# Kernel tuning notes

Measured on AMD Instinct MI355X. Metric: run time of the kernel, lower is better.

The kernel has to match this reference:

```python
import jax, jax.numpy as jnp
import numpy as np

B, T, DIN, H = 8, 512, 256, 512
D = 2 * H            # d_model = 1024
HEADS, DH, DEPTH, M = 8, 128, 2, 256  # M = nb_features
FF = 4 * D
KEPS = 1e-4          # performer kernel epsilon


def setup_inputs() -> dict:
    key = jax.random.key(0)
    ks = iter(jax.random.split(key, 64))
    def nrm(shape, s=1.0):
        return jax.random.normal(next(ks), shape, jnp.float32) * s
    inp = {"x": nrm((B, T, DIN))}
    # BiLSTM params, stacked over direction [2, ...]; torch gate order i,f,g,o
    for l, din in ((0, DIN), (1, D)):
        s = 1.0 / np.sqrt(H)
        inp[f"l{l}_Wih"] = nrm((2, 4 * H, din), s)
        inp[f"l{l}_Whh"] = nrm((2, 4 * H, H), s)
        inp[f"l{l}_bih"] = nrm((2, 4 * H), s)
        inp[f"l{l}_bhh"] = nrm((2, 4 * H), s)
    # FAVOR+ random projection (buffer), [nb_features, dim_head]
    inp["proj"] = nrm((M, DH))
    sd = 1.0 / np.sqrt(D)
    inp["ln1_g"] = jnp.ones((DEPTH, D)); inp["ln1_b"] = jnp.zeros((DEPTH, D))
    for n in ("Wq", "Wk", "Wv", "Wo"):
        inp[n] = nrm((DEPTH, D, D), sd)
    for n in ("bq", "bk", "bv", "bo"):
        inp[n] = jnp.zeros((DEPTH, D))
    inp["ln2_g"] = jnp.ones((DEPTH, D)); inp["ln2_b"] = jnp.zeros((DEPTH, D))
    inp["Wf1"] = nrm((DEPTH, D, FF), sd); inp["bf1"] = jnp.zeros((DEPTH, FF))
    inp["Wf2"] = nrm((DEPTH, FF, D), 1.0 / np.sqrt(FF)); inp["bf2"] = jnp.zeros((DEPTH, D))
    inp["cW1"] = nrm((D, H), sd); inp["cb1"] = jnp.zeros((H,))
    inp["cW2"] = nrm((H, 2), 1.0 / np.sqrt(H)); inp["cb2"] = jnp.zeros((2,))
    return inp


def _lstm_dir(x, Wih, Whh, bih, bhh, reverse):
    xs = jnp.swapaxes(x, 0, 1)                      # [T,B,Din]
    h0 = jnp.zeros((x.shape[0], H), x.dtype)
    def step(carry, xt):
        h, c = carry
        z = xt @ Wih.T + h @ Whh.T + bih + bhh      # [B,4H]
        i, f, g, o = jnp.split(z, 4, axis=-1)
        c = jax.nn.sigmoid(f) * c + jax.nn.sigmoid(i) * jnp.tanh(g)
        h = jax.nn.sigmoid(o) * jnp.tanh(c)
        return (h, c), h
    _, hs = jax.lax.scan(step, (h0, h0), xs, reverse=reverse)
    return jnp.swapaxes(hs, 0, 1)                   # [B,T,H], time-aligned


def _bilstm(x, Wih, Whh, bih, bhh):
    fwd = _lstm_dir(x, Wih[0], Whh[0], bih[0], bhh[0], False)
    bwd = _lstm_dir(x, Wih[1], Whh[1], bih[1], bhh[1], True)
    return jnp.concatenate([fwd, bwd], axis=-1)     # [B,T,2H]


def _ln(x, g, b):
    mu = jnp.mean(x, -1, keepdims=True)
    v = jnp.mean((x - mu) ** 2, -1, keepdims=True)
    return (x - mu) * jax.lax.rsqrt(v + 1e-5) * g + b


def _favor(data, proj, is_query):
    # softmax_kernel of performer-pytorch (eval mode, fixed projection)
    dn = DH ** -0.25
    dd = jnp.einsum('bhnd,md->bhnm', data * dn, proj)
    diag = jnp.sum(data * data, -1) * (dn * dn * 0.5)      # [b,h,n]
    if is_query:
        mx = jnp.max(dd, axis=-1, keepdims=True)
    else:
        mx = jnp.max(dd, axis=(-1, -2), keepdims=True)
    return (jnp.exp(dd - diag[..., None] - mx) + KEPS) * (M ** -0.5)


def _heads(x, W, b):
    return (x @ W + b).reshape(B, T, HEADS, DH).transpose(0, 2, 1, 3)


def reference(x, l0_Wih, l0_Whh, l0_bih, l0_bhh, l1_Wih, l1_Whh, l1_bih, l1_bhh,
              proj, ln1_g, ln1_b, Wq, bq, Wk, bk, Wv, bv, Wo, bo,
              ln2_g, ln2_b, Wf1, bf1, Wf2, bf2, cW1, cb1, cW2, cb2):
    h = _bilstm(x, l0_Wih, l0_Whh, l0_bih, l0_bhh)
    h = _bilstm(h, l1_Wih, l1_Whh, l1_bih, l1_bhh)          # [B,T,D]
    for i in range(DEPTH):
        # pre-norm FAVOR+ self-attention, non-causal linear attention
        y = _ln(h, ln1_g[i], ln1_b[i])
        q = _favor(_heads(y, Wq[i], bq[i]), proj, True)     # [b,h,n,m]
        k = _favor(_heads(y, Wk[i], bk[i]), proj, False)
        v = _heads(y, Wv[i], bv[i])                         # [b,h,n,d]
        dinv = 1.0 / jnp.einsum('bhnm,bhm->bhn', q, k.sum(axis=2))
        ctx = jnp.einsum('bhnm,bhnd->bhmd', k, v)
        o = jnp.einsum('bhnm,bhmd->bhnd', q, ctx) * dinv[..., None]
        o = o.transpose(0, 2, 1, 3).reshape(B, T, D)
        h = h + (o @ Wo[i] + bo[i])
        # pre-norm feedforward (GELU, mult 4)
        y = _ln(h, ln2_g[i], ln2_b[i])
        h = h + (jax.nn.gelu(y @ Wf1[i] + bf1[i], approximate=False) @ Wf2[i] + bf2[i])
    pooled = h.mean(axis=1)                                 # [B,D]
    logits = jax.nn.relu(pooled @ cW1 + cb1) @ cW2 + cb2    # [B,2]
    return logits
```

## Files before the change

### kernel.cpp

```cpp
#include <hip/hip_runtime.h>

#define KEPS 1e-4f

typedef __attribute__((ext_vector_type(8))) short bf16x8;
typedef __attribute__((ext_vector_type(4))) float f32x4;
typedef __attribute__((ext_vector_type(4))) unsigned u32x4;
typedef unsigned short u16;

__device__ float g_z0[2u*512*2048*8];
__device__ float g_z1[2u*512*2048*8];
__device__ float g_hres[8u*512*1024];
__device__ float g_qlin[8u*8*512*128];
__device__ float g_klin[8u*8*512*128];
__device__ float g_vlin[8u*8*512*128];
__device__ float g_qp[8u*8*512*256];
__device__ float g_ddb[8u*8*512*256];
__device__ float g_kT[8u*8*256*512];
__device__ float g_ctx[64u*256*128];
__device__ float g_bs0[2*2048];
__device__ float g_bs1[2*2048];
__device__ float g_diagq[32768];
__device__ float g_diagk[32768];
__device__ float g_kmx[64];
__device__ float g_ksum[64*256];
__device__ float g_dinv[32768];
__device__ __align__(16) unsigned g_hbuf[2*2*8*256];
__device__ float g_pooled[8*1024];

__device__ u16 g_xbf[8u*512*256];
__device__ u16 g_x1bf[8u*512*1024];
__device__ u16 g_ybf[8u*512*1024];
__device__ u16 g_ylo[8u*512*1024];
__device__ u16 g_obufbf[8u*512*1024];
__device__ u16 g_ffbbf[8u*512*4096];
__device__ u16 g_qhi[8u*8*512*128];
__device__ u16 g_qlo2[8u*8*512*128];
__device__ u16 g_khi[8u*8*512*128];
__device__ u16 g_klo2[8u*8*512*128];
__device__ u16 g_wih0b[2u*2048*256];
__device__ u16 g_wih1b[2u*2048*1024];
__device__ u16 g_wvt[2u*1024*1024];
__device__ u16 g_wot[2u*1024*1024];
__device__ u16 g_wf1t[2u*4096*1024];
__device__ u16 g_wf2t[2u*1024*4096];
__device__ u16 g_wqth[2u*1024*1024];
__device__ u16 g_wqtl[2u*1024*1024];
__device__ u16 g_wkth[2u*1024*1024];
__device__ u16 g_wktl[2u*1024*1024];
__device__ u16 g_projh[256*128];
__device__ u16 g_projl[256*128];

__device__ __forceinline__ float gelu_f(float x) {
  return 0.5f * x * (1.f + erff(x * 0.70710678118654752f));
}
__device__ __forceinline__ unsigned f2bf(float f) {
  unsigned x = __float_as_uint(f);
  return (x + 0x7FFFu + ((x >> 16) & 1u)) >> 16;
}
__device__ __forceinline__ float bf2f(unsigned h) {
  return __uint_as_float(h << 16);
}
__device__ __forceinline__ u32x4 ld16_sc1(const unsigned* p) {
  u32x4 v;
  asm volatile("global_load_dwordx4 %0, %1, off sc1\n\ts_waitcnt vmcnt(0)"
               : "=v"(v) : "v"(p) : "memory");
  return v;
}
__device__ __forceinline__ void st16_sc1(unsigned* p, u32x4 v) {
  asm volatile("global_store_dwordx4 %0, %1, off sc1" :: "v"(p), "v"(v) : "memory");
}

__global__ void k_add2(float* __restrict__ dst, const float* __restrict__ a,
                       const float* __restrict__ b, int n) {
  int i = blockIdx.x * 256 + threadIdx.x;
  if (i < n) dst[i] = a[i] + b[i];
}
__global__ void k_cvt(const float* __restrict__ src, u16* __restrict__ dst, int n4) {
  int i = blockIdx.x * 256 + threadIdx.x;
  if (i < n4) {
    float4 v = ((const float4*)src)[i];
    ushort4 o; o.x=(u16)f2bf(v.x); o.y=(u16)f2bf(v.y); o.z=(u16)f2bf(v.z); o.w=(u16)f2bf(v.w);
    ((ushort4*)dst)[i] = o;
  }
}
__global__ void k_scale_split(const float* __restrict__ a, u16* __restrict__ dh,
                              u16* __restrict__ dl, float s, int n) {
  int i = blockIdx.x*256 + threadIdx.x;
  if (i < n) {
    float v = a[i]*s;
    unsigned h = f2bf(v);
    dh[i] = (u16)h; dl[i] = (u16)f2bf(v - bf2f(h));
  }
}
__global__ void k_w2bfT(const float* __restrict__ src, u16* __restrict__ dst,
                        int K, int N, long long sBS, long long dBS)
{
  __shared__ float tile[32][33];
  const int z = blockIdx.z;
  const int n0 = blockIdx.x*32, k0 = blockIdx.y*32;
  const int tx = threadIdx.x, ty = threadIdx.y;
  const float* s = src + (long long)z*sBS;
  u16* d = dst + (long long)z*dBS;
  #pragma unroll
  for (int j = 0; j < 4; ++j)
    tile[ty + j*8][tx] = s[(long long)(k0 + ty + j*8)*N + n0 + tx];
  __syncthreads();
  #pragma unroll
  for (int j = 0; j < 4; ++j)
    d[(long long)(n0 + ty + j*8)*K + k0 + tx] = (u16)f2bf(tile[tx][ty + j*8]);
}
__global__ void k_w2bfT_split(const float* __restrict__ src, u16* __restrict__ dh,
                              u16* __restrict__ dl, int K, int N,
                              long long sBS, long long dBS)
{
  __shared__ float tile[32][33];
  const int z = blockIdx.z;
  const int n0 = blockIdx.x*32, k0 = blockIdx.y*32;
  const int tx = threadIdx.x, ty = threadIdx.y;
  const float* s = src + (long long)z*sBS;
  #pragma unroll
  for (int j = 0; j < 4; ++j)
    tile[ty + j*8][tx] = s[(long long)(k0 + ty + j*8)*N + n0 + tx];
  __syncthreads();
  #pragma unroll
  for (int j = 0; j < 4; ++j) {
    const float v = tile[tx][ty + j*8];
    const unsigned h = f2bf(v);
    const long long off = (long long)z*dBS + (long long)(n0 + ty + j*8)*K + k0 + tx;
    dh[off] = (u16)h; dl[off] = (u16)f2bf(v - bf2f(h));
  }
}

template<int MODE>
__global__ __launch_bounds__(256)
void k_bgemm(const u16* __restrict__ A, const u16* __restrict__ Bw,
             const float* __restrict__ bias, void* __restrict__ Cv,
             int Ndim, int Kdim,
             long long aBS, long long bBS, long long cBS, long long biasBS)
{
  __shared__ __align__(16) u16 As[128*40];
  __shared__ __align__(16) u16 Bs[128*40];
  const int tid = threadIdx.x;
  const int m0 = blockIdx.y * 128, n0 = blockIdx.x * 128, z = blockIdx.z;
  const u16* Ab = A + (long long)z*aBS;
  const u16* Bb = Bw + (long long)z*bBS;
  const int wv = tid >> 6, l = tid & 63;
  const int wm = wv >> 1, wn = wv & 1;
  const int lr = l & 15, lk = l >> 4;
  const int str = tid >> 2, stc = (tid & 3)*8;
  f32x4 acc[4][4];
  #pragma unroll
  for (int i=0;i<4;++i)
    #pragma unroll
    for (int j=0;j<4;++j) acc[i][j] = (f32x4){0.f,0.f,0.f,0.f};

  for (int k0 = 0; k0 < Kdim; k0 += 32) {
    #pragma unroll
    for (int q = 0; q < 2; ++q) {
      const int r = q*64 + str;
      *(uint4*)&As[r*40 + stc] = *(const uint4*)&Ab[(long long)(m0 + r)*Kdim + k0 + stc];
      *(uint4*)&Bs[r*40 + stc] = *(const uint4*)&Bb[(long long)(n0 + r)*Kdim + k0 + stc];
    }
    __syncthreads();
    bf16x8 af[4], bfr[4];
    #pragma unroll
    for (int i=0;i<4;++i) af[i]  = *(bf16x8*)&As[(wm*64 + i*16 + lr)*40 + lk*8];
    #pragma unroll
    for (int j=0;j<4;++j) bfr[j] = *(bf16x8*)&Bs[(wn*64 + j*16 + lr)*40 + lk*8];
    #pragma unroll
    for (int i=0;i<4;++i)
      #pragma unroll
      for (int j=0;j<4;++j)
        acc[i][j] = __builtin_amdgcn_mfma_f32_16x16x32_bf16(af[i], bfr[j], acc[i][j], 0, 0, 0);
    __syncthreads();
  }

  #pragma unroll
  for (int j=0;j<4;++j) {
    const int n = n0 + wn*64 + j*16 + lr;
    const float bvv = bias ? bias[(long long)z*biasBS + n] : 0.f;
    #pragma unroll
    for (int i=0;i<4;++i) {
      #pragma unroll
      for (int r=0;r<4;++r) {
        const int m = m0 + wm*64 + i*16 + lk*4 + r;
        float v = acc[i][j][r] + bvv;
        if (MODE == 0) {
          ((float*)Cv)[(long long)z*cBS + (long long)m*Ndim + n] = v;
        } else if (MODE == 1) {
          const int b_ = m >> 9, t_ = m & 511;
          ((float*)Cv)[(long long)z*cBS + ((long long)t_*2048 + n)*8 + b_] = v;
        } else if (MODE == 2) {
          const int b_ = m >> 9, t_ = m & 511;
          const int hd = n >> 7;
          ((float*)Cv)[(((long long)(b_*8 + hd))*512 + t_)*128 + (n & 127)] = v;
        } else if (MODE == 3) {
          float* cp = (float*)Cv + (long long)m*Ndim + n;
          *cp += v;
        } else if (MODE == 4) {
          ((u16*)Cv)[(long long)m*Ndim + n] = (u16)f2bf(gelu_f(v));
        }
      }
    }
  }
}

template<int MODE>
__global__ __launch_bounds__(256)
void k_b3gemm(const u16* __restrict__ Ah, const u16* __restrict__ Al,
              const u16* __restrict__ Bh, const u16* __restrict__ Bl,
              const float* __restrict__ bias, float* __restrict__ Cf,
              u16* __restrict__ Chi, u16* __restrict__ Clo,
              int Ndim, int Kdim)
{
  __shared__ __align__(16) u16 Ash[128*40];
  __shared__ __align__(16) u16 Asl[128*40];
  __shared__ __align__(16) u16 Bsh[128*40];
  __shared__ __align__(16) u16 Bsl[128*40];
  const int tid = threadIdx.x;
  const int m0 = blockIdx.y * 128, n0 = blockIdx.x * 128;
  const int wv = tid >> 6, l = tid & 63;
  const int wm = wv >> 1, wn = wv & 1;
  const int lr = l & 15, lk = l >> 4;
  const int str = tid >> 2, stc = (tid & 3)*8;
  f32x4 acc[4][4];
  #pragma unroll
  for (int i=0;i<4;++i)
    #pragma unroll
    for (int j=0;j<4;++j) acc[i][j] = (f32x4){0.f,0.f,0.f,0.f};

  for (int k0 = 0; k0 < Kdim; k0 += 32) {
    #pragma unroll
    for (int q = 0; q < 2; ++q) {
      const int r = q*64 + str;
      const long long ao = (long long)(m0 + r)*Kdim + k0 + stc;
      const long long bo = (long long)(n0 + r)*Kdim + k0 + stc;
      *(uint4*)&Ash[r*40 + stc] = *(const uint4*)&Ah[ao];
      *(uint4*)&Asl[r*40 + stc] = *(const uint4*)&Al[ao];
      *(uint4*)&Bsh[r*40 + stc] = *(const uint4*)&Bh[bo];
      *(uint4*)&Bsl[r*40 + stc] = *(const uint4*)&Bl[bo];
    }
    __syncthreads();
    bf16x8 ah[4], al_[4], bh[4], bl_[4];
    #pragma unroll
    for (int i=0;i<4;++i) {
      ah[i]  = *(bf16x8*)&Ash[(wm*64 + i*16 + lr)*40 + lk*8];
      al_[i] = *(bf16x8*)&Asl[(wm*64 + i*16 + lr)*40 + lk*8];
    }
    #pragma unroll
    for (int j=0;j<4;++j) {
      bh[j]  = *(bf16x8*)&Bsh[(wn*64 + j*16 + lr)*40 + lk*8];
      bl_[j] = *(bf16x8*)&Bsl[(wn*64 + j*16 + lr)*40 + lk*8];
    }
    #pragma unroll
    for (int i=0;i<4;++i)
      #pragma unroll
      for (int j=0;j<4;++j) {
        acc[i][j] = __builtin_amdgcn_mfma_f32_16x16x32_bf16(ah[i],  bh[j],  acc[i][j], 0, 0, 0);
        acc[i][j] = __builtin_amdgcn_mfma_f32_16x16x32_bf16(ah[i],  bl_[j], acc[i][j], 0, 0, 0);
        acc[i][j] = __builtin_amdgcn_mfma_f32_16x16x32_bf16(al_[i], bh[j],  acc[i][j], 0, 0, 0);
      }
    __syncthreads();
  }

  #pragma unroll
  for (int j=0;j<4;++j) {
    const int n = n0 + wn*64 + j*16 + lr;
    const float bvv = bias ? bias[n] : 0.f;
    #pragma unroll
    for (int i=0;i<4;++i) {
      #pragma unroll
      for (int r=0;r<4;++r) {
        const int m = m0 + wm*64 + i*16 + lk*4 + r;
        float v = acc[i][j][r] + bvv;
        if (MODE == 0) {
          Cf[(long long)m*Ndim + n] = v;
        } else if (MODE == 2) {
          const int b_ = m >> 9, t_ = m & 511;
          const int hd = n >> 7;
          const long long off = (((long long)(b_*8 + hd))*512 + t_)*128 + (n & 127);
          Cf[off] = v;
          const unsigned h = f2bf(v);
          Chi[off] = (u16)h;
          Clo[off] = (u16)f2bf(v - bf2f(h));
        }
      }
    }
  }
}

template<int BT, int MODE>
__global__ __launch_bounds__(256)
void k_gemm(const float* __restrict__ A, const float* __restrict__ Bw,
            const float* __restrict__ bias, float* __restrict__ C,
            int Mdim, int Ndim, int Kdim,
            long long aBS, long long bBS, long long cBS, long long biasBS,
            const float* __restrict__ aux)
{
  __shared__ float As[16][128];
  __shared__ float Bs[16][128];
  const int tid = threadIdx.x;
  const int tx = tid & 15, ty = tid >> 4;
  const int m0 = blockIdx.y * 128, n0 = blockIdx.x * 128;
  const int z = blockIdx.z;
  const float* Ab = A + (long long)z * aBS;
// ... 20 lines not shown
      #pragma unroll
      for (int l0 = 0; l0 < 512; l0 += 256) {
        const int ll = l0 + tid;
        const int kr = ll >> 5, n4 = (ll & 31) * 4;
        *(float4*)&Bs[kr][n4] = *(const float4*)&Bb[(long long)(k0 + kr) * Ndim + n0 + n4];
      }
    }
    __syncthreads();
    #pragma unroll
    for (int kk = 0; kk < 16; ++kk) {
      float4 af0 = *(const float4*)&As[kk][ty*4];
      float4 af1 = *(const float4*)&As[kk][64 + ty*4];
      float4 bf0 = *(const float4*)&Bs[kk][tx*4];
      float4 bf1 = *(const float4*)&Bs[kk][64 + tx*4];
      float av[8] = {af0.x,af0.y,af0.z,af0.w,af1.x,af1.y,af1.z,af1.w};
      float bv[8] = {bf0.x,bf0.y,bf0.z,bf0.w,bf1.x,bf1.y,bf1.z,bf1.w};
      #pragma unroll
      for (int i = 0; i < 8; ++i)
        #pragma unroll
        for (int j = 0; j < 8; ++j)
          acc[i][j] = fmaf(av[i], bv[j], acc[i][j]);
    }
    __syncthreads();
  }

  float* Cz = C + (long long)z * cBS;
  #pragma unroll
  for (int i = 0; i < 8; ++i) {
    const int m = m0 + ((i < 4) ? (ty*4 + i) : (64 + ty*4 + (i - 4)));
    #pragma unroll
    for (int jb = 0; jb < 2; ++jb) {
      const int ci = n0 + (jb ? 64 : 0) + tx*4;
      float4 v;
      v.x = acc[i][jb*4+0]; v.y = acc[i][jb*4+1];
      v.z = acc[i][jb*4+2]; v.w = acc[i][jb*4+3];
      if (MODE == 0) {
        *(float4*)&Cz[(long long)m * Ndim + ci] = v;
      } else if (MODE == 5) {
        const int b_ = z >> 3, hd = z & 7;
        const float sc = aux[(long long)z*512 + m];
        u16* Cb = (u16*)C;
        const long long off = ((long long)(b_*512 + m))*1024 + hd*128 + ci;
        Cb[off+0] = (u16)f2bf(v.x*sc);
        Cb[off+1] = (u16)f2bf(v.y*sc);
        Cb[off+2] = (u16)f2bf(v.z*sc);
        Cb[off+3] = (u16)f2bf(v.w*sc);
      }
    }
  }
}

template<int OBF>
__global__ __launch_bounds__(512)
void k_lstm5(const float* __restrict__ Z, const float* __restrict__ Whh,
             float* __restrict__ outf, u16* __restrict__ outb,
             unsigned* __restrict__ hbufU)
{
  extern __shared__ char smem[];
  short*          Wl    = (short*)smem;
  short*          hl    = (short*)(smem + 131072);
  float*          gates = (float*)(smem + 139264);
  unsigned short* houts = (unsigned short*)(smem + 143360);

  const int slice = blockIdx.x & 15, dir = blockIdx.x >> 4;
  const int tid = threadIdx.x;
  const int u0 = slice * 32;

  for (int blk = tid; blk < 8192; blk += 512) {
    const int lr2 = blk >> 6, bi = blk & 63;
    const long long src = ((long long)dir*2048 + (lr2>>5)*512 + u0 + (lr2&31))*512 + bi*8;
    float4 w0 = *(const float4*)&Whh[src];
    float4 w1 = *(const float4*)&Whh[src + 4];
    unsigned* dst = (unsigned*)&Wl[lr2*512 + (((bi + lr2) & 63) << 3)];
    dst[0] = f2bf(w0.x) | (f2bf(w0.y) << 16);
    dst[1] = f2bf(w0.z) | (f2bf(w0.w) << 16);
    dst[2] = f2bf(w1.x) | (f2bf(w1.y) << 16);
    dst[3] = f2bf(w1.z) | (f2bf(w1.w) << 16);
  }
  for (int i = tid; i < 2048; i += 512) ((unsigned*)hl)[i] = 0u;

  const int wv = tid >> 6, l = tid & 63;
  const int arow = wv*16 + (l & 15);
  const int bb   = l & 7;
  const int qoff = l >> 4;
  const int jj = tid >> 3, bcomb = tid & 7;
  float cst = 0.f;
  int gt = 1;
  int pt = 2;

  for (int s = 0; s < 512; ++s) {
    const int t = dir ? (511 - s) : s;
    float z0v = 0.f, z1v = 0.f, z2v = 0.f, z3v = 0.f;
    if (tid < 256) {
      const float* zp = Z + (((long long)dir*512 + t)*16384) + (u0 + jj)*8 + bcomb;
      z0v = zp[0]; z1v = zp[4096]; z2v = zp[8192]; z3v = zp[12288];
    }
    if (s > 0) {
      const unsigned base = ((unsigned)((s & 1)*2 + dir)) * 2048;
      const unsigned* src = &hbufU[base + tid*4];
      u32x4 v;
      for (;;) {
        v = ld16_sc1(src);
        const int tag = (int)((v.x & 1u) | (((v.x >> 16) & 1u) << 1) | ((v.y & 1u) << 2));
        if (tag == gt) break;
      }
      const int b = tid >> 6, q = tid & 63;
      *(u32x4*)((char*)hl + b*1024 + (((q + b) & 63) << 4)) = v;
    }
    __syncthreads();
    f32x4 acc0 = {0.f,0.f,0.f,0.f}, acc1 = {0.f,0.f,0.f,0.f};
    #pragma unroll
    for (int ks = 0; ks < 8; ++ks) {
      const int qa = (2*ks)*4 + qoff, qb = (2*ks + 1)*4 + qoff;
      bf16x8 a0 = *(bf16x8*)&Wl[arow*512 + (((qa + arow) & 63) << 3)];
      bf16x8 b0 = *(bf16x8*)&hl[bb*512   + (((qa + bb)   & 63) << 3)];
      acc0 = __builtin_amdgcn_mfma_f32_16x16x32_bf16(a0, b0, acc0, 0, 0, 0);
      bf16x8 a1 = *(bf16x8*)&Wl[arow*512 + (((qb + arow) & 63) << 3)];
      bf16x8 b1 = *(bf16x8*)&hl[bb*512   + (((qb + bb)   & 63) << 3)];
      acc1 = __builtin_amdgcn_mfma_f32_16x16x32_bf16(a1, b1, acc1, 0, 0, 0);
    }
    const int bcol = l & 15;
    if (bcol < 8) {
      #pragma unroll
      for (int r = 0; r < 4; ++r)
        gates[(wv*16 + qoff*4 + r)*8 + bcol] = acc0[r] + acc1[r];
    }
    __syncthreads();
    if (tid < 256) {
      const float gi = gates[jj*8        + bcomb] + z0v;
      const float gf = gates[(32+jj)*8   + bcomb] + z1v;
      const float gg = gates[(64+jj)*8   + bcomb] + z2v;
      const float go = gates[(96+jj)*8   + bcomb] + z3v;
      const float ig = 1.f/(1.f + expf(-gi));
      const float fg = 1.f/(1.f + expf(-gf));
      const float og = 1.f/(1.f + expf(-go));
      cst = fg*cst + ig*tanhf(gg);
      const float hv = og*tanhf(cst);
      const unsigned hb = f2bf(hv);
      if (OBF) outb[((long long)(bcomb*512 + t))*1024 + (dir<<9) + u0 + jj] = (u16)hb;
      else     outf[((long long)(bcomb*512 + t))*1024 + (dir<<9) + u0 + jj] = hv;
      houts[bcomb*32 + jj] = (unsigned short)hb;
    }
    __syncthreads();
    if (s != 511 && tid < 32) {
      const int b = tid >> 2, q4 = tid & 3;
      u32x4 w = *(const u32x4*)&houts[b*32 + q4*8];
      w.x = (w.x & ~0x00010001u) | (unsigned)(pt & 1) | (((unsigned)(pt >> 1) & 1u) << 16);
      w.y = (w.y & ~1u) | ((unsigned)(pt >> 2) & 1u);
      const unsigned base2 = ((unsigned)(((s+1) & 1)*2 + dir)) * 2048;
      st16_sc1(&hbufU[base2 + b*256 + (u0 >> 1) + q4*4], w);
    }
    gt = (gt == 7) ? 1 : gt + 1;
    pt = (pt == 7) ? 1 : pt + 1;
  }
}

__global__ __launch_bounds__(256)
void k_ln(const float* __restrict__ X, const float* __restrict__ gw,
          const float* __restrict__ bw, u16* __restrict__ Yh, u16* __restrict__ Yl)
{
  const int row = blockIdx.x, tid = threadIdx.x;
  const float* xr = X + (long long)row * 1024;
  float4 v = *(const float4*)&xr[tid*4];
  float s  = v.x + v.y + v.z + v.w;
  float ss = v.x*v.x + v.y*v.y + v.z*v.z + v.w*v.w;
  #pragma unroll
  for (int off = 1; off < 64; off <<= 1) {
    s  += __shfl_xor(s, off, 64);
    ss += __shfl_xor(ss, off, 64);
  }
  __shared__ float rs[4], rss[4];
  const int w = tid >> 6;
  if ((tid & 63) == 0) { rs[w] = s; rss[w] = ss; }
  __syncthreads();
  s  = rs[0] + rs[1] + rs[2] + rs[3];
  ss = rss[0] + rss[1] + rss[2] + rss[3];
  const float mu = s * (1.f/1024.f);
  const float var = ss * (1.f/1024.f) - mu*mu;
  const float rstd = rsqrtf(var + 1e-5f);
  float4 g4 = *(const float4*)&gw[tid*4];
  float4 b4 = *(const float4*)&bw[tid*4];
  float4 o;
  o.x = (v.x - mu)*rstd*g4.x + b4.x;
  o.y = (v.y - mu)*rstd*g4.y + b4.y;
  o.z = (v.z - mu)*rstd*g4.z + b4.z;
  o.w = (v.w - mu)*rstd*g4.w + b4.w;
  ushort4 hh, ll;
  hh.x=(u16)f2bf(o.x); ll.x=(u16)f2bf(o.x - bf2f(f2bf(o.x)));
  hh.y=(u16)f2bf(o.y); ll.y=(u16)f2bf(o.y - bf2f(f2bf(o.y)));
  hh.z=(u16)f2bf(o.z); ll.z=(u16)f2bf(o.z - bf2f(f2bf(o.z)));
  hh.w=(u16)f2bf(o.w); ll.w=(u16)f2bf(o.w - bf2f(f2bf(o.w)));
  *(ushort4*)&Yh[(long long)row*1024 + tid*4] = hh;
  *(ushort4*)&Yl[(long long)row*1024 + tid*4] = ll;
}

__global__ void k_diag(const float* __restrict__ X, float* __restrict__ dout)
{
  const int tid = threadIdx.x;
  const int row = blockIdx.x*4 + (tid >> 6);
  const int lane = tid & 63;
  float2 v = *(const float2*)&X[(long long)row*128 + lane*2];
  float ss = v.x*v.x + v.y*v.y;
  #pragma unroll
  for (int off = 1; off < 64; off <<= 1) ss += __shfl_xor(ss, off, 64);
  if (lane == 0) dout[row] = ss * 0.044194173824159216f;
}

// ... 152 lines not shown
  const float* ln2b  = (const float*)d_in[21];
  const float* Wf1   = (const float*)d_in[22];
  const float* bf1   = (const float*)d_in[23];
  const float* Wf2   = (const float*)d_in[24];
  const float* bf2   = (const float*)d_in[25];
  const float* cW1   = (const float*)d_in[26];
  const float* cb1   = (const float*)d_in[27];
  const float* cW2   = (const float*)d_in[28];
  const float* cb2   = (const float*)d_in[29];

  float* z0    = (float*)symp(HIP_SYMBOL(g_z0));
  float* z1    = (float*)symp(HIP_SYMBOL(g_z1));
  float* hres  = (float*)symp(HIP_SYMBOL(g_hres));
  float* qlin  = (float*)symp(HIP_SYMBOL(g_qlin));
  float* klin  = (float*)symp(HIP_SYMBOL(g_klin));
  float* vlin  = (float*)symp(HIP_SYMBOL(g_vlin));
  float* qp    = (float*)symp(HIP_SYMBOL(g_qp));
  float* ddb   = (float*)symp(HIP_SYMBOL(g_ddb));
  float* kT    = (float*)symp(HIP_SYMBOL(g_kT));
  float* ctx   = (float*)symp(HIP_SYMBOL(g_ctx));
  float* bs0   = (float*)symp(HIP_SYMBOL(g_bs0));
  float* bs1   = (float*)symp(HIP_SYMBOL(g_bs1));
  float* diagq = (float*)symp(HIP_SYMBOL(g_diagq));
  float* diagk = (float*)symp(HIP_SYMBOL(g_diagk));
  float* kmx   = (float*)symp(HIP_SYMBOL(g_kmx));
  float* ksum  = (float*)symp(HIP_SYMBOL(g_ksum));
  float* dinv  = (float*)symp(HIP_SYMBOL(g_dinv));
  unsigned* hbuf = (unsigned*)symp(HIP_SYMBOL(g_hbuf));
  float* pooled= (float*)symp(HIP_SYMBOL(g_pooled));
  u16* xbf   = (u16*)symp(HIP_SYMBOL(g_xbf));
  u16* x1bf  = (u16*)symp(HIP_SYMBOL(g_x1bf));
  u16* ybf   = (u16*)symp(HIP_SYMBOL(g_ybf));
  u16* ylo   = (u16*)symp(HIP_SYMBOL(g_ylo));
  u16* obufbf= (u16*)symp(HIP_SYMBOL(g_obufbf));
  u16* ffbbf = (u16*)symp(HIP_SYMBOL(g_ffbbf));
  u16* qhi   = (u16*)symp(HIP_SYMBOL(g_qhi));
  u16* qlo2  = (u16*)symp(HIP_SYMBOL(g_qlo2));
  u16* khi   = (u16*)symp(HIP_SYMBOL(g_khi));
  u16* klo2  = (u16*)symp(HIP_SYMBOL(g_klo2));
  u16* wih0b = (u16*)symp(HIP_SYMBOL(g_wih0b));
  u16* wih1b = (u16*)symp(HIP_SYMBOL(g_wih1b));
  u16* wvt   = (u16*)symp(HIP_SYMBOL(g_wvt));
  u16* wot   = (u16*)symp(HIP_SYMBOL(g_wot));
  u16* wf1t  = (u16*)symp(HIP_SYMBOL(g_wf1t));
  u16* wf2t  = (u16*)symp(HIP_SYMBOL(g_wf2t));
  u16* wqth  = (u16*)symp(HIP_SYMBOL(g_wqth));
  u16* wqtl  = (u16*)symp(HIP_SYMBOL(g_wqtl));
  u16* wkth  = (u16*)symp(HIP_SYMBOL(g_wkth));
  u16* wktl  = (u16*)symp(HIP_SYMBOL(g_wktl));
  u16* projh = (u16*)symp(HIP_SYMBOL(g_projh));
  u16* projl = (u16*)symp(HIP_SYMBOL(g_projl));

  const float dn = 0.29730177875068026f;
  const int LSTM_LDS = 143872;
  (void)hipFuncSetAttribute((const void*)k_lstm5<1>,
                            hipFuncAttributeMaxDynamicSharedMemorySize, LSTM_LDS);
  (void)hipFuncSetAttribute((const void*)k_lstm5<0>,
                            hipFuncAttributeMaxDynamicSharedMemorySize, LSTM_LDS);

  k_add2<<<16, 256, 0, stream>>>(bs0, l0bih, l0bhh, 4096);
  k_add2<<<16, 256, 0, stream>>>(bs1, l1bih, l1bhh, 4096);
  k_scale_split<<<128, 256, 0, stream>>>(proj, projh, projl, dn, 32768);

  k_cvt<<<1024, 256, 0, stream>>>(x, xbf, 262144);
  k_cvt<<<1024, 256, 0, stream>>>(l0Wih, wih0b, 262144);
  k_cvt<<<4096, 256, 0, stream>>>(l1Wih, wih1b, 1048576);
  k_w2bfT<<<dim3(32,32,2),  dim3(32,8), 0, stream>>>(Wv,  wvt,  1024, 1024, 1048576LL, 1048576LL);
  k_w2bfT<<<dim3(32,32,2),  dim3(32,8), 0, stream>>>(Wo,  wot,  1024, 1024, 1048576LL, 1048576LL);
  k_w2bfT<<<dim3(128,32,2), dim3(32,8), 0, stream>>>(Wf1, wf1t, 1024, 4096, 4194304LL, 4194304LL);
  k_w2bfT<<<dim3(32,128,2), dim3(32,8), 0, stream>>>(Wf2, wf2t, 4096, 1024, 4194304LL, 4194304LL);
  k_w2bfT_split<<<dim3(32,32,2), dim3(32,8), 0, stream>>>(Wq, wqth, wqtl, 1024, 1024, 1048576LL, 1048576LL);
  k_w2bfT_split<<<dim3(32,32,2), dim3(32,8), 0, stream>>>(Wk, wkth, wktl, 1024, 1024, 1048576LL, 1048576LL);

  k_bgemm<1><<<dim3(16,32,2), 256, 0, stream>>>(xbf, wih0b, bs0, z0,
      2048, 256, 0LL, 524288LL, 8388608LL, 2048LL);
  k_lstm5<1><<<32, 512, LSTM_LDS, stream>>>(z0, l0Whh, nullptr, x1bf, hbuf);
  k_bgemm<1><<<dim3(16,32,2), 256, 0, stream>>>(x1bf, wih1b, bs1, z1,
      2048, 1024, 0LL, 2097152LL, 8388608LL, 2048LL);
  k_lstm5<0><<<32, 512, LSTM_LDS, stream>>>(z1, l1Whh, hres, nullptr, hbuf);

  for (int i = 0; i < 2; ++i) {
    const long long wOffU = (long long)i * 1048576;
    k_ln<<<4096, 256, 0, stream>>>(hres, ln1g + i*1024, ln1b + i*1024, ybf, ylo);
    k_b3gemm<2><<<dim3(8,32,1), 256, 0, stream>>>(ybf, ylo, wqth + wOffU, wqtl + wOffU,
        bq + i*1024, qlin, qhi, qlo2, 1024, 1024);
    k_b3gemm<2><<<dim3(8,32,1), 256, 0, stream>>>(ybf, ylo, wkth + wOffU, wktl + wOffU,
        bk + i*1024, klin, khi, klo2, 1024, 1024);
    k_bgemm<2><<<dim3(8,32,1), 256, 0, stream>>>(ybf, wvt + wOffU, bv + i*1024, vlin,
        1024, 1024, 0LL, 0LL, 0LL, 0LL);
    k_diag<<<8192, 256, 0, stream>>>(qlin, diagq);
    k_diag<<<8192, 256, 0, stream>>>(klin, diagk);
    k_b3gemm<0><<<dim3(2,256,1), 256, 0, stream>>>(qhi, qlo2, projh, projl,
        nullptr, qp, nullptr, nullptr, 256, 128);
    k_favq<<<8192, 256, 0, stream>>>(qp, diagq);
    k_b3gemm<0><<<dim3(2,256,1), 256, 0, stream>>>(khi, klo2, projh, projl,
        nullptr, ddb, nullptr, nullptr, 256, 128);
    k_kmax<<<64, 256, 0, stream>>>(ddb, kmx);
    k_fkT<<<dim3(16,8,64), dim3(32,8), 0, stream>>>(ddb, diagk, kmx, kT);
    k_ksum<<<4096, 256, 0, stream>>>(kT, ksum);
    k_gemm<0,0><<<dim3(1,2,64), 256, 0, stream>>>(kT, vlin, nullptr, ctx,
        256, 128, 512, 131072LL, 65536LL, 32768LL, 0LL, nullptr);
    k_dinv<<<8192, 256, 0, stream>>>(qp, ksum, dinv);
    k_gemm<0,5><<<dim3(1,4,64), 256, 0, stream>>>(qp, ctx, nullptr, (float*)obufbf,
        512, 128, 256, 131072LL, 32768LL, 0LL, 0LL, dinv);
    k_bgemm<3><<<dim3(8,32,1), 256, 0, stream>>>(obufbf, wot + wOffU, bo + i*1024, hres,
        1024, 1024, 0LL, 0LL, 0LL, 0LL);
    k_ln<<<4096, 256, 0, stream>>>(hres, ln2g + i*1024, ln2b + i*1024, ybf, ylo);
    k_bgemm<4><<<dim3(32,32,1), 256, 0, stream>>>(ybf, wf1t + (long long)i*4194304,
        bf1 + i*4096, ffbbf, 4096, 1024, 0LL, 0LL, 0LL, 0LL);
    k_bgemm<3><<<dim3(8,32,1), 256, 0, stream>>>(ffbbf, wf2t + (long long)i*4194304,
        bf2 + i*1024, hres, 1024, 4096, 0LL, 0LL, 0LL, 0LL);
  }

  k_pool<<<32, 256, 0, stream>>>(hres, pooled);
  k_cls<<<8, 256, 0, stream>>>(pooled, cW1, cb1, cW2, cb2, (float*)d_out);
}
```

Baseline: 4.362 ms.

## Split LSTM batch into two halves to overlap h exchange with MFMA

The recurrent LSTM kernel now splits the 8 batch columns into two groups of 4, each with its own LDS h buffer and its own global exchange slot. While one half's gate matmul and cell update run, the other half's hidden state load from peer blocks is already in flight. The z loads and h loads are issued early with raw asm and waited on with explicit vmcnt counts, and plain s_barrier replaces __syncthreads. This is meant to hide cross-block communication latency on the serial time chain, at the cost of doubling the MFMA passes, which now use half-empty operands, and of fragile hand-managed waitcnt ordering.

```diff
diff --git a/kernel.cpp b/kernel.cpp
--- a/kernel.cpp
+++ b/kernel.cpp
@@ -24,7 +24,7 @@
 __device__ float g_kmx[64];
 __device__ float g_ksum[64*256];
 __device__ float g_dinv[32768];
-__device__ __align__(16) unsigned g_hbuf[2*2*8*256];
+__device__ __align__(16) unsigned g_hbuf[2*2*2*1024];
 __device__ float g_pooled[8*1024];
 
 __device__ u16 g_xbf[8u*512*256];
@@ -66,8 +66,20 @@
                : "=v"(v) : "v"(p) : "memory");
   return v;
 }
+__device__ __forceinline__ void ld16_sc1_issue(u32x4& v, const unsigned* p) {
+  asm volatile("global_load_dwordx4 %0, %1, off sc1" : "=v"(v) : "v"(p));
+}
+__device__ __forceinline__ void ld4_issue(float& d, const float* p) {
+  asm volatile("global_load_dword %0, %1, off" : "=v"(d) : "v"(p));
+}
 __device__ __forceinline__ void st16_sc1(unsigned* p, u32x4 v) {
   asm volatile("global_store_dwordx4 %0, %1, off sc1" :: "v"(p), "v"(v) : "memory");
+}
+__device__ __forceinline__ void bar_raw() {
+  asm volatile("s_waitcnt lgkmcnt(0)" ::: "memory");
+  __builtin_amdgcn_sched_barrier(0);
+  __builtin_amdgcn_s_barrier();
+  __builtin_amdgcn_sched_barrier(0);
 }
 
 __global__ void k_add2(float* __restrict__ dst, const float* __restrict__ a,
@@ -377,15 +389,15 @@
 
 template<int OBF>
 __global__ __launch_bounds__(512)
-void k_lstm5(const float* __restrict__ Z, const float* __restrict__ Whh,
+void k_lstm6(const float* __restrict__ Z, const float* __restrict__ Whh,
              float* __restrict__ outf, u16* __restrict__ outb,
              unsigned* __restrict__ hbufU)
 {
   extern __shared__ char smem[];
-  short*          Wl    = (short*)smem;
-  short*          hl    = (short*)(smem + 131072);
-  float*          gates = (float*)(smem + 139264);
-  unsigned short* houts = (unsigned short*)(smem + 143360);
+  short* Wl    = (short*)smem;
+  char*  hlA   = smem + 131072;
+  char*  hlB   = smem + 135168;
+  float* gates = (float*)(smem + 139264);
 
   const int slice = blockIdx.x & 15, dir = blockIdx.x >> 4;
   const int tid = threadIdx.x;
@@ -402,82 +414,166 @@
     dst[2] = f2bf(w1.x) | (f2bf(w1.y) << 16);
     dst[3] = f2bf(w1.z) | (f2bf(w1.w) << 16);
   }
-  for (int i = tid; i < 2048; i += 512) ((unsigned*)hl)[i] = 0u;
+  for (int i = tid; i < 2048; i += 512) {
+    ((unsigned*)hlA)[i & 1023] = 0u;
+    ((unsigned*)hlB)[(i >> 1) & 1023] = 0u;
+  }
+  for (int i = tid; i < 1024; i += 512) { ((unsigned*)hlA)[i] = 0u; ((unsigned*)hlB)[i] = 0u; }
 
   const int wv = tid >> 6, l = tid & 63;
   const int arow = wv*16 + (l & 15);
-  const int bb   = l & 7;
+  const int bbop = l & 3;
   const int qoff = l >> 4;
-  const int jj = tid >> 3, bcomb = tid & 7;
+  const int cidx = tid & 127, jjc = cidx >> 2, bloc = cidx & 3;
+  const int isA = (tid < 128), isB = (tid >= 128 && tid < 256);
+  const int batch = isA ? bloc : 4 + bloc;
+  const int q4 = 2*((cidx >> 6) & 1) + ((l >> 5) & 1);
   float cst = 0.f;
   int gt = 1;
   int pt = 2;
+  u32x4 vA = {0,0,0,0}, vB = {0,0,0,0};
+
+  const int dirbase = dir * 2;
 
   for (int s = 0; s < 512; ++s) {
     const int t = dir ? (511 - s) : s;
-    float z0v = 0.f, z1v = 0.f, z2v = 0.f, z3v = 0.f;
+    float z0v=0.f, z1v=0.f, z2v=0.f, z3v=0.f;
+    const float* zp = Z + (((long long)dir*512 + t)*16384) + (u0 + jjc)*8 + batch;
     if (tid < 256) {
-      const float* zp = Z + (((long long)dir*512 + t)*16384) + (u0 + jj)*8 + bcomb;
-      z0v = zp[0]; z1v = zp[4096]; z2v = zp[8192]; z3v = zp[12288];
-    }
-    if (s > 0) {
-      const unsigned base = ((unsigned)((s & 1)*2 + dir)) * 2048;
-      const unsigned* src = &hbufU[base + tid*4];
-      u32x4 v;
-      for (;;) {
-        v = ld16_sc1(src);
-        const int tag = (int)((v.x & 1u) | (((v.x >> 16) & 1u) << 1) | ((v.y & 1u) << 2));
-        if (tag == gt) break;
+      ld4_issue(z0v, zp);
+      ld4_issue(z1v, zp + 4096);
+      ld4_issue(z2v, zp + 8192);
+      ld4_issue(z3v, zp + 12288);
+    }
+    const unsigned* adA = hbufU + (((s & 1)*2 + dir)*2 + 0)*1024 + tid*4;
+    if (s > 0 && tid < 256) {
+      asm volatile("s_waitcnt vmcnt(4)" : "+v"(vA));
+      int tag = (int)((vA.x & 1u) | (((vA.x >> 16) & 1u) << 1) | ((vA.y & 1u) << 2));
+      while (tag != gt) {
+        vA = ld16_sc1(adA);
+        tag = (int)((vA.x & 1u) | (((vA.x >> 16) & 1u) << 1) | ((vA.y & 1u) << 2));
       }
       const int b = tid >> 6, q = tid & 63;
-      *(u32x4*)((char*)hl + b*1024 + (((q + b) & 63) << 4)) = v;
-    }
-    __syncthreads();
-    f32x4 acc0 = {0.f,0.f,0.f,0.f}, acc1 = {0.f,0.f,0.f,0.f};
-    #pragma unroll
-    for (int ks = 0; ks < 8; ++ks) {
-      const int qa = (2*ks)*4 + qoff, qb = (2*ks + 1)*4 + qoff;
-      bf16x8 a0 = *(bf16x8*)&Wl[arow*512 + (((qa + arow) & 63) << 3)];
-      bf16x8 b0 = *(bf16x8*)&hl[bb*512   + (((qa + bb)   & 63) << 3)];
-      acc0 = __builtin_amdgcn_mfma_f32_16x16x32_bf16(a0, b0, acc0, 0, 0, 0);
-      bf16x8 a1 = *(bf16x8*)&Wl[arow*512 + (((qb + arow) & 63) << 3)];
-      bf16x8 b1 = *(bf16x8*)&hl[bb*512   + (((qb + bb)   & 63) << 3)];
-      acc1 = __builtin_amdgcn_mfma_f32_16x16x32_bf16(a1, b1, acc1, 0, 0, 0);
-    }
-    const int bcol = l & 15;
-    if (bcol < 8) {
+      *(u32x4*)(hlA + b*1024 + (((q + b) & 63) << 4)) = vA;
+    }
+    const unsigned* adB = hbufU + (((s & 1)*2 + dir)*2 + 1)*1024 + tid*4;
+    if (s > 0 && tid < 256) ld16_sc1_issue(vB, adB);
+    bar_raw();
+    {
+      f32x4 acc0 = {0.f,0.f,0.f,0.f}, acc1 = {0.f,0.f,0.f,0.f};
       #pragma unroll
-      for (int r = 0; r < 4; ++r)
-        gates[(wv*16 + qoff*4 + r)*8 + bcol] = acc0[r] + acc1[r];
-    }
-    __syncthreads();
-    if (tid < 256) {
-      const float gi = gates[jj*8        + bcomb] + z0v;
-      const float gf = gates[(32+jj)*8   + bcomb] + z1v;
-      const float gg = gates[(64+jj)*8   + bcomb] + z2v;
-      const float go = gates[(96+jj)*8   + bcomb] + z3v;
+      for (int ks = 0; ks < 8; ++ks) {
+        const int qa = (2*ks)*4 + qoff, qb = (2*ks + 1)*4 + qoff;
+        bf16x8 a0 = *(bf16x8*)&Wl[arow*512 + (((qa + arow) & 63) << 3)];
+        bf16x8 b0 = *(bf16x8*)(hlA + bbop*1024 + (((qa + bbop) & 63) << 4));
+        acc0 = __builtin_amdgcn_mfma_f32_16x16x32_bf16(a0, b0, acc0, 0, 0, 0);
+        bf16x8 a1 = *(bf16x8*)&Wl[arow*512 + (((qb + arow) & 63) << 3)];
+        bf16x8 b1 = *(bf16x8*)(hlA + bbop*1024 + (((qb + bbop) & 63) << 4));
+        acc1 = __builtin_amdgcn_mfma_f32_16x16x32_bf16(a1, b1, acc1, 0, 0, 0);
+      }
+      const int bcol = l & 15;
+      if (bcol < 4) {
+        #pragma unroll
+        for (int r = 0; r < 4; ++r)
+          gates[(wv*16 + qoff*4 + r)*4 + bcol] = acc0[r] + acc1[r];
+      }
+    }
+    bar_raw();
+    if (isA) {
+      if (s == 0) { asm volatile("s_waitcnt vmcnt(0)" : "+v"(z0v), "+v"(z1v), "+v"(z2v), "+v"(z3v)); }
+      else        { asm volatile("s_waitcnt vmcnt(1)" : "+v"(z0v), "+v"(z1v), "+v"(z2v), "+v"(z3v)); }
+      const float gi = gates[jjc*4 + bloc]        + z0v;
+      const float gf = gates[(32+jjc)*4 + bloc]   + z1v;
+      const float gg = gates[(64+jjc)*4 + bloc]   + z2v;
+      const float go = gates[(96+jjc)*4 + bloc]   + z3v;
       const float ig = 1.f/(1.f + expf(-gi));
       const float fg = 1.f/(1.f + expf(-gf));
       const float og = 1.f/(1.f + expf(-go));
       cst = fg*cst + ig*tanhf(gg);
       const float hv = og*tanhf(cst);
       const unsigned hb = f2bf(hv);
-      if (OBF) outb[((long long)(bcomb*512 + t))*1024 + (dir<<9) + u0 + jj] = (u16)hb;
-      else     outf[((long long)(bcomb*512 + t))*1024 + (dir<<9) + u0 + jj] = hv;
-      houts[bcomb*32 + jj] = (unsigned short)hb;
-    }
-    __syncthreads();
-    if (s != 511 && tid < 32) {
-      const int b = tid >> 2, q4 = tid & 3;
-      u32x4 w = *(const u32x4*)&houts[b*32 + q4*8];
-      w.x = (w.x & ~0x00010001u) | (unsigned)(pt & 1) | (((unsigned)(pt >> 1) & 1u) << 16);
-      w.y = (w.y & ~1u) | ((unsigned)(pt >> 2) & 1u);
-      const unsigned base2 = ((unsigned)(((s+1) & 1)*2 + dir)) * 2048;
-      st16_sc1(&hbufU[base2 + b*256 + (u0 >> 1) + q4*4], w);
+      if (OBF) outb[((long long)(batch*512 + t))*1024 + (dir<<9) + u0 + jjc] = (u16)hb;
+      else     outf[((long long)(batch*512 + t))*1024 + (dir<<9) + u0 + jjc] = hv;
+      unsigned p  = hb | (((unsigned)__shfl_down((int)hb, 4)) << 16);
+      unsigned q0 = p, q1 = (unsigned)__shfl_down((int)p, 8);
+      unsigned r2 = (unsigned)__shfl_down((int)q0, 16), r3 = (unsigned)__shfl_down((int)q1, 16);
+      if (s != 511 && (l & 28) == 0) {
+        u32x4 w;
+        w.x = (q0 & ~0x00010001u) | (unsigned)(pt & 1) | (((unsigned)(pt >> 1) & 1u) << 16);
+        w.y = (q1 & ~1u) | ((unsigned)(pt >> 2) & 1u);
+        w.z = r2; w.w = r3;
+        unsigned* pa = hbufU + ((((s+1) & 1)*2 + dir)*2 + 0)*1024 + bloc*256 + (u0 >> 1) + q4*4;
+        st16_sc1(pa, w);
+      }
+    }
+    if (tid < 256) {
+      if (s > 0) {
+        asm volatile("s_waitcnt vmcnt(0)" : "+v"(vB), "+v"(z0v), "+v"(z1v), "+v"(z2v), "+v"(z3v));
+        int tag = (int)((vB.x & 1u) | (((vB.x >> 16) & 1u) << 1) | ((vB.y & 1u) << 2));
+        while (tag != gt) {
+          vB = ld16_sc1(adB);
+          tag = (int)((vB.x & 1u) | (((vB.x >> 16) & 1u) << 1) | ((vB.y & 1u) << 2));
+        }
+        const int b = tid >> 6, q = tid & 63;
+        *(u32x4*)(hlB + b*1024 + (((q + b) & 63) << 4)) = vB;
+      } else {
+        asm volatile("s_waitcnt vmcnt(0)" : "+v"(z0v), "+v"(z1v), "+v"(z2v), "+v"(z3v));
+      }
+    }
+    bar_raw();
+    {
+      f32x4 acc0 = {0.f,0.f,0.f,0.f}, acc1 = {0.f,0.f,0.f,0.f};
+      #pragma unroll
+      for (int ks = 0; ks < 8; ++ks) {
+        const int qa = (2*ks)*4 + qoff, qb = (2*ks + 1)*4 + qoff;
+        bf16x8 a0 = *(bf16x8*)&Wl[arow*512 + (((qa + arow) & 63) << 3)];
+        bf16x8 b0 = *(bf16x8*)(hlB + bbop*1024 + (((qa + bbop) & 63) << 4));
+        acc0 = __builtin_amdgcn_mfma_f32_16x16x32_bf16(a0, b0, acc0, 0, 0, 0);
+        bf16x8 a1 = *(bf16x8*)&Wl[arow*512 + (((qb + arow) & 63) << 3)];
+        bf16x8 b1 = *(bf16x8*)(hlB + bbop*1024 + (((qb + bbop) & 63) << 4));
+        acc1 = __builtin_amdgcn_mfma_f32_16x16x32_bf16(a1, b1, acc1, 0, 0, 0);
+      }
+      const int bcol = l & 15;
+      if (bcol < 4) {
+        #pragma unroll
+        for (int r = 0; r < 4; ++r)
+          gates[(wv*16 + qoff*4 + r)*4 + bcol] = acc0[r] + acc1[r];
+      }
+    }
+    bar_raw();
+    if (isB) {
+      const float gi = gates[jjc*4 + bloc]        + z0v;
+      const float gf = gates[(32+jjc)*4 + bloc]   + z1v;
+      const float gg = gates[(64+jjc)*4 + bloc]   + z2v;
+      const float go = gates[(96+jjc)*4 + bloc]   + z3v;
+      const float ig = 1.f/(1.f + expf(-gi));
+      const float fg = 1.f/(1.f + expf(-gf));
+      const float og = 1.f/(1.f + expf(-go));
+      cst = fg*cst + ig*tanhf(gg);
+      const float hv = og*tanhf(cst);
+      const unsigned hb = f2bf(hv);
+      if (OBF) outb[((long long)(batch*512 + t))*1024 + (dir<<9) + u0 + jjc] = (u16)hb;
+      else     outf[((long long)(batch*512 + t))*1024 + (dir<<9) + u0 + jjc] = hv;
+      unsigned p  = hb | (((unsigned)__shfl_down((int)hb, 4)) << 16);
+      unsigned q0 = p, q1 = (unsigned)__shfl_down((int)p, 8);
+      unsigned r2 = (unsigned)__shfl_down((int)q0, 16), r3 = (unsigned)__shfl_down((int)q1, 16);
+      if (s != 511 && (l & 28) == 0) {
+        u32x4 w;
+        w.x = (q0 & ~0x00010001u) | (unsigned)(pt & 1) | (((unsigned)(pt >> 1) & 1u) << 16);
+        w.y = (q1 & ~1u) | ((unsigned)(pt >> 2) & 1u);
+        w.z = r2; w.w = r3;
+        unsigned* pa = hbufU + ((((s+1) & 1)*2 + dir)*2 + 1)*1024 + bloc*256 + (u0 >> 1) + q4*4;
+        st16_sc1(pa, w);
+      }
+    }
+    if (s < 511 && tid < 256) {
+      const unsigned* adA2 = hbufU + ((((s+1) & 1)*2 + dir)*2 + 0)*1024 + tid*4;
+      ld16_sc1_issue(vA, adA2);
     }
     gt = (gt == 7) ? 1 : gt + 1;
     pt = (pt == 7) ? 1 : pt + 1;
   }
+  (void)dirbase;
 }
 
 __global__ __launch_bounds__(256)
@@ -736,10 +832,10 @@
   u16* projl = (u16*)symp(HIP_SYMBOL(g_projl));
 
   const float dn = 0.29730177875068026f;
-  const int LSTM_LDS = 143872;
-  (void)hipFuncSetAttribute((const void*)k_lstm5<1>,
+  const int LSTM_LDS = 141312;
+  (void)hipFuncSetAttribute((const void*)k_lstm6<1>,
                             hipFuncAttributeMaxDynamicSharedMemorySize, LSTM_LDS);
-  (void)hipFuncSetAttribute((const void*)k_lstm5<0>,
+  (void)hipFuncSetAttribute((const void*)k_lstm6<0>,
                             hipFuncAttributeMaxDynamicSharedMemorySize, LSTM_LDS);
 
   k_add2<<<16, 256, 0, stream>>>(bs0, l0bih, l0bhh, 4096);
@@ -758,10 +854,10 @@
 
   k_bgemm<1><<<dim3(16,32,2), 256, 0, stream>>>(xbf, wih0b, bs0, z0,
       2048, 256, 0LL, 524288LL, 8388608LL, 2048LL);
-  k_lstm5<1><<<32, 512, LSTM_LDS, stream>>>(z0, l0Whh, nullptr, x1bf, hbuf);
+  k_lstm6<1><<<32, 512, LSTM_LDS, stream>>>(z0, l0Whh, nullptr, x1bf, hbuf);
   k_bgemm<1><<<dim3(16,32,2), 256, 0, stream>>>(x1bf, wih1b, bs1, z1,
       2048, 1024, 0LL, 2097152LL, 8388608LL, 2048LL);
-  k_lstm5<0><<<32, 512, LSTM_LDS, stream>>>(z1, l1Whh, hres, nullptr, hbuf);
+  k_lstm6<0><<<32, 512, LSTM_LDS, stream>>>(z1, l1Whh, hres, nullptr, hbuf);
 
   for (int i = 0; i < 2; ++i) {
     const long long wOffU = (long long)i * 1048576;
```

Measured after the change: 6.422 ms. 1.47x slower.

## Use direct global-to-LDS loads in GEMMs and trim LSTM step barriers

Applied to the files above, without the earlier changes.

The bf16 GEMM kernels now stage tiles with global_load_lds straight into unpadded LDS instead of going through registers, so each wave fills a contiguous 32-row block. In the recurrent LSTM kernel, the per-step hidden-state publish now packs bf16 outputs with wave shuffles and stores them directly. This drops the houts staging buffer and one __syncthreads per timestep. The other barriers become raw s_barrier calls that wait only on LDS counters. The risks are LDS bank conflicts from removing the row padding, and subtle ordering issues from the weaker barriers.

```diff
diff --git a/kernel.cpp b/kernel.cpp
--- a/kernel.cpp
+++ b/kernel.cpp
@@ -69,6 +69,17 @@
 __device__ __forceinline__ void st16_sc1(unsigned* p, u32x4 v) {
   asm volatile("global_store_dwordx4 %0, %1, off sc1" :: "v"(p), "v"(v) : "memory");
 }
+__device__ __forceinline__ void bar_raw() {
+  asm volatile("s_waitcnt lgkmcnt(0)" ::: "memory");
+  __builtin_amdgcn_sched_barrier(0);
+  __builtin_amdgcn_s_barrier();
+  __builtin_amdgcn_sched_barrier(0);
+}
+__device__ __forceinline__ void gll16(const void* g, void* l) {
+  __builtin_amdgcn_global_load_lds(
+      (const __attribute__((address_space(1))) void*)g,
+      (__attribute__((address_space(3))) void*)l, 16, 0, 0);
+}
 
 __global__ void k_add2(float* __restrict__ dst, const float* __restrict__ a,
                        const float* __restrict__ b, int n) {
@@ -138,8 +149,8 @@
              int Ndim, int Kdim,
              long long aBS, long long bBS, long long cBS, long long biasBS)
 {
-  __shared__ __align__(16) u16 As[128*40];
-  __shared__ __align__(16) u16 Bs[128*40];
+  __shared__ __align__(16) u16 As[128*32];
+  __shared__ __align__(16) u16 Bs[128*32];
   const int tid = threadIdx.x;
   const int m0 = blockIdx.y * 128, n0 = blockIdx.x * 128, z = blockIdx.z;
   const u16* Ab = A + (long long)z*aBS;
@@ -147,7 +158,7 @@
   const int wv = tid >> 6, l = tid & 63;
   const int wm = wv >> 1, wn = wv & 1;
   const int lr = l & 15, lk = l >> 4;
-  const int str = tid >> 2, stc = (tid & 3)*8;
+  const int lrow = l >> 2, lkq = (l & 3)*8;
   f32x4 acc[4][4];
   #pragma unroll
   for (int i=0;i<4;++i)
@@ -157,16 +168,16 @@
   for (int k0 = 0; k0 < Kdim; k0 += 32) {
     #pragma unroll
     for (int q = 0; q < 2; ++q) {
-      const int r = q*64 + str;
-      *(uint4*)&As[r*40 + stc] = *(const uint4*)&Ab[(long long)(m0 + r)*Kdim + k0 + stc];
-      *(uint4*)&Bs[r*40 + stc] = *(const uint4*)&Bb[(long long)(n0 + r)*Kdim + k0 + stc];
+      const int r = wv*32 + q*16 + lrow;
+      gll16(&Ab[(long long)(m0 + r)*Kdim + k0 + lkq], &As[(wv*32 + q*16)*32]);
+      gll16(&Bb[(long long)(n0 + r)*Kdim + k0 + lkq], &Bs[(wv*32 + q*16)*32]);
     }
     __syncthreads();
     bf16x8 af[4], bfr[4];
     #pragma unroll
-    for (int i=0;i<4;++i) af[i]  = *(bf16x8*)&As[(wm*64 + i*16 + lr)*40 + lk*8];
-    #pragma unroll
-    for (int j=0;j<4;++j) bfr[j] = *(bf16x8*)&Bs[(wn*64 + j*16 + lr)*40 + lk*8];
+    for (int i=0;i<4;++i) af[i]  = *(bf16x8*)&As[(wm*64 + i*16 + lr)*32 + lk*8];
+    #pragma unroll
+    for (int j=0;j<4;++j) bfr[j] = *(bf16x8*)&Bs[(wn*64 + j*16 + lr)*32 + lk*8];
     #pragma unroll
     for (int i=0;i<4;++i)
       #pragma unroll
@@ -213,16 +224,16 @@
               u16* __restrict__ Chi, u16* __restrict__ Clo,
               int Ndim, int Kdim)
 {
-  __shared__ __align__(16) u16 Ash[128*40];
-  __shared__ __align__(16) u16 Asl[128*40];
-  __shared__ __align__(16) u16 Bsh[128*40];
-  __shared__ __align__(16) u16 Bsl[128*40];
+  __shared__ __align__(16) u16 Ash[128*32];
+  __shared__ __align__(16) u16 Asl[128*32];
+  __shared__ __align__(16) u16 Bsh[128*32];
+  __shared__ __align__(16) u16 Bsl[128*32];
   const int tid = threadIdx.x;
   const int m0 = blockIdx.y * 128, n0 = blockIdx.x * 128;
   const int wv = tid >> 6, l = tid & 63;
   const int wm = wv >> 1, wn = wv & 1;
   const int lr = l & 15, lk = l >> 4;
-  const int str = tid >> 2, stc = (tid & 3)*8;
+  const int lrow = l >> 2, lkq = (l & 3)*8;
   f32x4 acc[4][4];
   #pragma unroll
   for (int i=0;i<4;++i)
@@ -232,25 +243,26 @@
   for (int k0 = 0; k0 < Kdim; k0 += 32) {
     #pragma unroll
     for (int q = 0; q < 2; ++q) {
-      const int r = q*64 + str;
-      const long long ao = (long long)(m0 + r)*Kdim + k0 + stc;
-      const long long bo = (long long)(n0 + r)*Kdim + k0 + stc;
-      *(uint4*)&Ash[r*40 + stc] = *(const uint4*)&Ah[ao];
-      *(uint4*)&Asl[r*40 + stc] = *(const uint4*)&Al[ao];
-      *(uint4*)&Bsh[r*40 + stc] = *(const uint4*)&Bh[bo];
-      *(uint4*)&Bsl[r*40 + stc] = *(const uint4*)&Bl[bo];
+      const int r = wv*32 + q*16 + lrow;
+      const long long ao = (long long)(m0 + r)*Kdim + k0 + lkq;
+      const long long bo = (long long)(n0 + r)*Kdim + k0 + lkq;
+      const int lb = (wv*32 + q*16)*32;
+      gll16(&Ah[ao], &Ash[lb]);
+      gll16(&Al[ao], &Asl[lb]);
+      gll16(&Bh[bo], &Bsh[lb]);
+      gll16(&Bl[bo], &Bsl[lb]);
     }
     __syncthreads();
     bf16x8 ah[4], al_[4], bh[4], bl_[4];
     #pragma unroll
     for (int i=0;i<4;++i) {
-      ah[i]  = *(bf16x8*)&Ash[(wm*64 + i*16 + lr)*40 + lk*8];
-      al_[i] = *(bf16x8*)&Asl[(wm*64 + i*16 + lr)*40 + lk*8];
+      ah[i]  = *(bf16x8*)&Ash[(wm*64 + i*16 + lr)*32 + lk*8];
+      al_[i] = *(bf16x8*)&Asl[(wm*64 + i*16 + lr)*32 + lk*8];
     }
     #pragma unroll
     for (int j=0;j<4;++j) {
-      bh[j]  = *(bf16x8*)&Bsh[(wn*64 + j*16 + lr)*40 + lk*8];
-      bl_[j] = *(bf16x8*)&Bsl[(wn*64 + j*16 + lr)*40 + lk*8];
+      bh[j]  = *(bf16x8*)&Bsh[(wn*64 + j*16 + lr)*32 + lk*8];
+      bl_[j] = *(bf16x8*)&Bsl[(wn*64 + j*16 + lr)*32 + lk*8];
     }
     #pragma unroll
     for (int i=0;i<4;++i)
@@ -377,15 +389,14 @@
 
 template<int OBF>
 __global__ __launch_bounds__(512)
-void k_lstm5(const float* __restrict__ Z, const float* __restrict__ Whh,
+void k_lstm7(const float* __restrict__ Z, const float* __restrict__ Whh,
              float* __restrict__ outf, u16* __restrict__ outb,
              unsigned* __restrict__ hbufU)
 {
   extern __shared__ char smem[];
-  short*          Wl    = (short*)smem;
-  short*          hl    = (short*)(smem + 131072);
-  float*          gates = (float*)(smem + 139264);
-  unsigned short* houts = (unsigned short*)(smem + 143360);
+  short*  Wl    = (short*)smem;
+  short*  hl    = (short*)(smem + 131072);
+  float*  gates = (float*)(smem + 139264);
 
   const int slice = blockIdx.x & 15, dir = blockIdx.x >> 4;
   const int tid = threadIdx.x;
@@ -432,7 +443,7 @@
       const int b = tid >> 6, q = tid & 63;
       *(u32x4*)((char*)hl + b*1024 + (((q + b) & 63) << 4)) = v;
     }
-    __syncthreads();
+    bar_raw();
     f32x4 acc0 = {0.f,0.f,0.f,0.f}, acc1 = {0.f,0.f,0.f,0.f};
     #pragma unroll
     for (int ks = 0; ks < 8; ++ks) {
@@ -450,7 +461,7 @@
       for (int r = 0; r < 4; ++r)
         gates[(wv*16 + qoff*4 + r)*8 + bcol] = acc0[r] + acc1[r];
     }
-    __syncthreads();
+    bar_raw();
     if (tid < 256) {
       const float gi = gates[jj*8        + bcomb] + z0v;
       const float gf = gates[(32+jj)*8   + bcomb] + z1v;
@@ -464,16 +475,18 @@
       const unsigned hb = f2bf(hv);
       if (OBF) outb[((long long)(bcomb*512 + t))*1024 + (dir<<9) + u0 + jj] = (u16)hb;
       else     outf[((long long)(bcomb*512 + t))*1024 + (dir<<9) + u0 + jj] = hv;
-      houts[bcomb*32 + jj] = (unsigned short)hb;
-    }
-    __syncthreads();
-    if (s != 511 && tid < 32) {
-      const int b = tid >> 2, q4 = tid & 3;
-      u32x4 w = *(const u32x4*)&houts[b*32 + q4*8];
-      w.x = (w.x & ~0x00010001u) | (unsigned)(pt & 1) | (((unsigned)(pt >> 1) & 1u) << 16);
-      w.y = (w.y & ~1u) | ((unsigned)(pt >> 2) & 1u);
-      const unsigned base2 = ((unsigned)(((s+1) & 1)*2 + dir)) * 2048;
-      st16_sc1(&hbufU[base2 + b*256 + (u0 >> 1) + q4*4], w);
+      unsigned p  = hb | (((unsigned)__shfl_down((int)hb, 8, 64)) << 16);
+      unsigned y1 = (unsigned)__shfl_down((int)p, 16, 64);
+      unsigned y2 = (unsigned)__shfl_down((int)p, 32, 64);
+      unsigned y3 = (unsigned)__shfl_down((int)p, 48, 64);
+      if (s != 511 && (l & 56) == 0) {
+        u32x4 w;
+        w.x = (p  & ~0x00010001u) | (unsigned)(pt & 1) | (((unsigned)(pt >> 1) & 1u) << 16);
+        w.y = (y1 & ~1u) | ((unsigned)(pt >> 2) & 1u);
+        w.z = y2; w.w = y3;
+        const unsigned base2 = ((unsigned)(((s+1) & 1)*2 + dir)) * 2048;
+        st16_sc1(&hbufU[base2 + bcomb*256 + (u0 >> 1) + wv*4], w);
+      }
     }
     gt = (gt == 7) ? 1 : gt + 1;
     pt = (pt == 7) ? 1 : pt + 1;
@@ -736,10 +749,10 @@
   u16* projl = (u16*)symp(HIP_SYMBOL(g_projl));
 
   const float dn = 0.29730177875068026f;
-  const int LSTM_LDS = 143872;
-  (void)hipFuncSetAttribute((const void*)k_lstm5<1>,
+  const int LSTM_LDS = 143360;
+  (void)hipFuncSetAttribute((const void*)k_lstm7<1>,
                             hipFuncAttributeMaxDynamicSharedMemorySize, LSTM_LDS);
-  (void)hipFuncSetAttribute((const void*)k_lstm5<0>,
+  (void)hipFuncSetAttribute((const void*)k_lstm7<0>,
                             hipFuncAttributeMaxDynamicSharedMemorySize, LSTM_LDS);
 
   k_add2<<<16, 256, 0, stream>>>(bs0, l0bih, l0bhh, 4096);
@@ -758,10 +771,10 @@
 
   k_bgemm<1><<<dim3(16,32,2), 256, 0, stream>>>(xbf, wih0b, bs0, z0,
       2048, 256, 0LL, 524288LL, 8388608LL, 2048LL);
-  k_lstm5<1><<<32, 512, LSTM_LDS, stream>>>(z0, l0Whh, nullptr, x1bf, hbuf);
+  k_lstm7<1><<<32, 512, LSTM_LDS, stream>>>(z0, l0Whh, nullptr, x1bf, hbuf);
   k_bgemm<1><<<dim3(16,32,2), 256, 0, stream>>>(x1bf, wih1b, bs1, z1,
       2048, 1024, 0LL, 2097152LL, 8388608LL, 2048LL);
-  k_lstm5<0><<<32, 512, LSTM_LDS, stream>>>(z1, l1Whh, hres, nullptr, hbuf);
+  k_lstm7<0><<<32, 512, LSTM_LDS, stream>>>(z1, l1Whh, hres, nullptr, hbuf);
 
   for (int i = 0; i < 2; ++i) {
     const long long wOffU = (long long)i * 1048576;
```

Result: slower. 5.284 ms (+21.1%).
